# Kernel tuning notes

Measured on AMD Instinct MI355X. Metric: run time of the kernel, lower is better.

The kernel has to match this reference:

```python
import jax, jax.numpy as jnp
import numpy as np

B, M, N, K = 2, 25000, 100000, 16
HID, DIM, NGROUPS = 64, 64, 8
GN_EPS = 1e-5


def conv1x1(x, w, b):
    # x: [B,C,M,K], w: [O,C], b: [O]
    return jnp.einsum('bcmk,oc->bomk', x, w) + b[None, :, None, None]


def group_norm(x, gamma, beta, ngroups):
    b, c, m, k = x.shape
    xg = x.reshape(b, ngroups, c // ngroups, m, k)
    mu = xg.mean(axis=(2, 3, 4), keepdims=True)
    var = xg.var(axis=(2, 3, 4), keepdims=True)
    xn = ((xg - mu) / jnp.sqrt(var + GN_EPS)).reshape(b, c, m, k)
    return xn * gamma[None, :, None, None] + beta[None, :, None, None]


def mlp(x, w1, b1, g, be, w2, b2):
    h = jax.nn.relu(group_norm(conv1x1(x, w1, b1), g, be, NGROUPS))
    return conv1x1(h, w2, b2)


def setup_inputs() -> dict:
    key = jax.random.key(0)
    ks = jax.random.split(key, 16)
    inp = {
        'q_xyzs': jax.random.normal(ks[0], (B, 3, M), jnp.float32),
        'k_xyzs': jax.random.normal(ks[1], (B, 3, N), jnp.float32),
        'knn_idx': jax.random.randint(ks[2], (B, M, K), 0, N),
        'mask': jax.random.randint(ks[3], (B, M, K), 0, 2).astype(bool),
        # embed_positions MLP params
        'pe_w1': jax.random.normal(ks[4], (HID, 4), jnp.float32) * 0.05,
        'pe_b1': jnp.zeros((HID,), jnp.float32),
        'pe_g': jnp.ones((HID,), jnp.float32),
        'pe_be': jnp.zeros((HID,), jnp.float32),
        'pe_w2': jax.random.normal(ks[5], (DIM, HID), jnp.float32) * 0.05,
        'pe_b2': jnp.zeros((DIM,), jnp.float32),
        # attention MLP params
        'at_w1': jax.random.normal(ks[6], (HID, DIM), jnp.float32) * 0.05,
        'at_b1': jnp.zeros((HID,), jnp.float32),
        'at_g': jnp.ones((HID,), jnp.float32),
        'at_be': jnp.zeros((HID,), jnp.float32),
        'at_w2': jax.random.normal(ks[7], (DIM, HID), jnp.float32) * 0.05,
        'at_b2': jnp.zeros((DIM,), jnp.float32),
    }
    return inp


def reference(q_xyzs, k_xyzs, knn_idx, mask,
              pe_w1, pe_b1, pe_g, pe_be, pe_w2, pe_b2,
              at_w1, at_b1, at_g, at_be, at_w2, at_b2):
    # gather KNN coordinates: [B,3,M,K]
    knn_xyzs = jax.vmap(lambda pts, idx: pts[:, idx])(k_xyzs, knn_idx)
    offset = knn_xyzs - q_xyzs[..., None]
    dist = jnp.linalg.norm(offset, axis=1, keepdims=True)  # [B,1,M,K]
    direction = offset / jnp.maximum(dist, 1e-12)
    local_pattern = jnp.concatenate([direction, dist], axis=1)  # [B,4,M,K]

    pe = mlp(local_pattern, pe_w1, pe_b1, pe_g, pe_be, pe_w2, pe_b2)  # [B,DIM,M,K]
    attn = mlp(pe, at_w1, at_b1, at_g, at_be, at_w2, at_b2)
    mask_value = -jnp.finfo(attn.dtype).max
    attn = jnp.where(mask[:, None], attn, mask_value)
    attn = jax.nn.softmax(attn, axis=-1)
    return (pe * attn).sum(axis=-1)  # [B,DIM,M]
```

## Files before the change

### kernel.cpp

```cpp
#include <hip/hip_runtime.h>

#define Bn 2
#define Mn 25000
#define Nn 100000
#define MK 400000
#define GN_EPS 1e-5f
#define NEG_BIG (-3.402823466e+38f)
#define LOG2E 1.44269504088896340736f

#define G1 512
#define G2 512

#define BEFF_OFF 0
#define B1P_OFF  64
#define AB1P_OFF 192
#define AB2L_OFF 320
#define WF16_OFF 384
#define AW1P_OFF 6528
#define W1F_OFF  10624
#define MSK_OFF  11136
#define SP_OFF   36160
#define YP_OFF   52544
#define YS_OFF   183616
#define KXT_OFF  184128
#define QT_OFF   984128
#define XF_OFF   1184128

typedef _Float16 hf8 __attribute__((ext_vector_type(8)));
typedef _Float16 hf4 __attribute__((ext_vector_type(4)));
typedef _Float16 hf2 __attribute__((ext_vector_type(2)));
typedef float f32x16 __attribute__((ext_vector_type(16)));

__device__ __forceinline__ f32x16 mfma16(hf8 a, hf8 b, f32x16 c) {
    return __builtin_amdgcn_mfma_f32_32x32x16_f16(a, b, c, 0, 0, 0);
}
__device__ __forceinline__ f32x16 splat16(float v) {
    f32x16 x;
#pragma unroll
    for (int r = 0; r < 16; ++r) x[r] = v;
    return x;
}
__device__ __forceinline__ hf8 zero8() {
    hf8 z;
#pragma unroll
    for (int j = 0; j < 8; ++j) z[j] = (_Float16)0.f;
    return z;
}
__device__ __forceinline__ hf2 pkcvt(float a, float b) {
    return __builtin_bit_cast(hf2, __builtin_amdgcn_cvt_pkrtz(a, b));
}
__device__ __forceinline__ hf2 pkrelu(hf2 v) {
    hf2 z; z[0] = (_Float16)0.f; z[1] = (_Float16)0.f;
    return __builtin_elementwise_max(v, z);
}
__device__ __forceinline__ float waveSum(float v) {
#pragma unroll
    for (int s = 32; s; s >>= 1) v += __shfl_down(v, s, 64);
    return v;
}
#define ROWFN(r, lane) (((r) & 3) + 8*((r) >> 2) + 4*((lane) >> 5))

__global__ __launch_bounds__(256) void prep0_kernel(
    const float* __restrict__ q, const float* __restrict__ kx,
    float* __restrict__ ws)
{
    float4* kxt = (float4*)(ws + KXT_OFF);
    float4* qt  = (float4*)(ws + QT_OFF);
    for (int e = blockIdx.x*256 + threadIdx.x; e < 2*Nn; e += gridDim.x*256) {
        const int b = e / Nn, n = e % Nn;
        float4 v;
        v.x = kx[(b*3+0)*Nn + n]; v.y = kx[(b*3+1)*Nn + n];
        v.z = kx[(b*3+2)*Nn + n]; v.w = 0.f;
        kxt[e] = v;
    }
    for (int e = blockIdx.x*256 + threadIdx.x; e < 2*Mn; e += gridDim.x*256) {
        const int b = e / Mn, m = e % Mn;
        float4 v;
        v.x = q[(b*3+0)*Mn + m]; v.y = q[(b*3+1)*Mn + m];
        v.z = q[(b*3+2)*Mn + m]; v.w = 0.f;
        qt[e] = v;
    }
}

__global__ __launch_bounds__(256) void gatherx_kernel(
    const int* __restrict__ idx, const int* __restrict__ mask,
    float* __restrict__ ws)
{
    __shared__ float red[4][16];
    const int b = blockIdx.y;
    const float4* kxt = (const float4*)(ws + KXT_OFF) + (size_t)b*Nn;
    const float4* qt  = (const float4*)(ws + QT_OFF)  + (size_t)b*Mn;
    _Float16* xf = (_Float16*)(ws + XF_OFF);
    unsigned short* m16 = (unsigned short*)(ws + MSK_OFF) + (size_t)b*25024;
    float v[14];
#pragma unroll
    for (int j = 0; j < 14; ++j) v[j] = 0.f;

    for (int i = blockIdx.x*256 + threadIdx.x; i < MK; i += G1*256) {
        const int mm = i >> 4;
        const int id = idx[(size_t)b*MK + i];
        const float4 kv = kxt[id];
        const float4 qv = qt[mm];
        const float ox = kv.x - qv.x, oy = kv.y - qv.y, oz = kv.z - qv.z;
        const float d  = sqrtf(ox*ox + oy*oy + oz*oz);
        const float inv = 1.0f / fmaxf(d, 1e-12f);
        const float x0 = ox*inv, x1 = oy*inv, x2 = oz*inv, x3 = d;

        const hf2 lo = pkcvt(x0, x1);
        const hf2 hi = pkcvt(x2, x3);
        hf4 pk;
        pk[0] = lo[0]; pk[1] = lo[1]; pk[2] = hi[0]; pk[3] = hi[1];
        *(hf4*)&xf[((size_t)b*MK + i)*4] = pk;

        const unsigned long long mb = __ballot(mask[(size_t)b*MK + i] != 0);
        if ((threadIdx.x & 63) == 0)
            *(unsigned long long*)&m16[i >> 4] = mb;

        v[0] += x0; v[1] += x1; v[2] += x2; v[3] += x3;
        v[4] += x0*x0; v[5] += x0*x1; v[6] += x0*x2; v[7] += x0*x3;
        v[8] += x1*x1; v[9] += x1*x2; v[10] += x1*x3;
        v[11] += x2*x2; v[12] += x2*x3; v[13] += x3*x3;
    }
    const int lane = threadIdx.x & 63, wv = threadIdx.x >> 6;
#pragma unroll
    for (int j = 0; j < 14; ++j) v[j] = waveSum(v[j]);
    if (lane == 0) {
#pragma unroll
        for (int j = 0; j < 14; ++j) red[wv][j] = v[j];
    }
    __syncthreads();
    if (threadIdx.x < 14)
        ws[SP_OFF + ((size_t)b*G1 + blockIdx.x)*16 + threadIdx.x] =
            red[0][threadIdx.x] + red[1][threadIdx.x] + red[2][threadIdx.x] + red[3][threadIdx.x];
}

__global__ void prep1_kernel(
    const float* __restrict__ ws_r,
    const float* __restrict__ w1, const float* __restrict__ b1,
    const float* __restrict__ g1, const float* __restrict__ be1,
    const float* __restrict__ w2, const float* __restrict__ pe_b2,
    const float* __restrict__ aw1, const float* __restrict__ ab1,
    const float* __restrict__ aw2, const float* __restrict__ ab2,
    float* __restrict__ ws)
{
    const int t = threadIdx.x;
    _Float16* WF = (_Float16*)(ws + WF16_OFF);

    if (blockIdx.x > 0) {
        const int e = (blockIdx.x - 1)*256 + t;
        const int o = e >> 6, c = e & 63;
        WF[e]        = (_Float16)w2[e];
        WF[4096 + e] = (_Float16)(aw2[e] * LOG2E);
        float acc = 0.f;
        for (int d = 0; d < 64; ++d) acc = fmaf(aw1[o*64 + d], w2[d*64 + c], acc);
        WF[8192 + e] = (_Float16)acc;
        return;
    }

    __shared__ double S[2][14];
    __shared__ float Eh[2][64], Eq[2][64];

    if (t < 28) {
        const int b = t / 14, j = t % 14;
        const float* p = ws_r + SP_OFF + (size_t)b*G1*16 + j;
        double acc = 0.0;
        for (int g = 0; g < G1; g += 4)
            acc += (double)p[(g+0)*16] + (double)p[(g+1)*16]
                 + (double)p[(g+2)*16] + (double)p[(g+3)*16];
        S[b][j] = acc;
    }
    __syncthreads();

    if (t < 128) {
        const int b = t >> 6, o = t & 63;
        const double inv = 1.0 / (double)MK;
        double mu[4];
#pragma unroll
        for (int c = 0; c < 4; ++c) mu[c] = S[b][c] * inv;
        double m2[4][4];
        {
            const int map[4][4] = {{0,1,2,3},{1,4,5,6},{2,5,7,8},{3,6,8,9}};
#pragma unroll
            for (int c = 0; c < 4; ++c)
#pragma unroll
                for (int c2 = 0; c2 < 4; ++c2)
                    m2[c][c2] = S[b][4 + map[c][c2]] * inv;
        }
        double w[4];
#pragma unroll
        for (int c = 0; c < 4; ++c) w[c] = (double)w1[o*4 + c];
        double s = 0.0, qd = 0.0;
#pragma unroll
        for (int c = 0; c < 4; ++c) {
            s += w[c] * mu[c];
#pragma unroll
            for (int c2 = 0; c2 < 4; ++c2) qd += w[c]*w[c2]*m2[c][c2];
        }
        const double bb = (double)b1[o];
        Eh[b][o] = (float)(s + bb);
        Eq[b][o] = (float)(qd + 2.0*bb*s + bb*bb);
    }
    __syncthreads();
    if (t < 128) {
        const int b = t >> 6, o = t & 63, g = o & ~7;
        float mg = 0.f, qg = 0.f;
#pragma unroll
        for (int j = 0; j < 8; ++j) { mg += Eh[b][g + j]; qg += Eq[b][g + j]; }
        mg *= 0.125f; qg *= 0.125f;
        const float var = fmaxf(qg - mg*mg, 0.f);
        const float a = g1[o] / sqrtf(var + GN_EPS);
        const float c1v = be1[o] - mg*a;
        _Float16* W1F = (_Float16*)(ws + W1F_OFF);
        hf8 wrow;
#pragma unroll
        for (int c = 0; c < 4; ++c) wrow[c] = (_Float16)(a * w1[o*4 + c]);
#pragma unroll
        for (int c = 4; c < 8; ++c) wrow[c] = (_Float16)0.f;
        *(hf8*)&W1F[(b*64 + o)*8] = wrow;
        ws[B1P_OFF + b*64 + o] = fmaf(a, b1[o], c1v);
    }
    if (t < 64) {
        float acc = ab1[t];
        for (int d = 0; d < 64; ++d) acc = fmaf(aw1[t*64 + d], pe_b2[d], acc);
        ws[BEFF_OFF + t] = acc;
    } else if (t < 128) {
        ws[AB2L_OFF + (t - 64)] = ab2[t - 64] * LOG2E;
    }
}

__global__ __launch_bounds__(256, 4) void pass2_kernel(
    const float* __restrict__ cws, float* __restrict__ ws)
{
    __shared__ __align__(16) _Float16 Xs[4][32][72];
    const int b = blockIdx.y;
    const int tid = threadIdx.x, lane = tid & 63, wv = tid >> 6;
    const int colA = lane & 31;
    const int klo = (lane >> 5) * 8;
    const _Float16* xf  = (const _Float16*)(cws + XF_OFF);
    const _Float16* WFe = (const _Float16*)(cws + WF16_OFF) + 8192;
    const _Float16* W1F = (const _Float16*)(cws + W1F_OFF);

    hf8 BW[2][4];
#pragma unroll
    for (int jc = 0; jc < 2; ++jc)
#pragma unroll
        for (int ks = 0; ks < 4; ++ks)
            BW[jc][ks] = *(const hf8*)&WFe[(2*colA + jc)*64 + 16*ks + klo];
    hf8 BX[2];
    if (klo == 0) {
        BX[0] = *(const hf8*)&W1F[(b*64 + 2*colA)*8];
        BX[1] = *(const hf8*)&W1F[(b*64 + 2*colA + 1)*8];
    } else { BX[0] = zero8(); BX[1] = zero8(); }
    const float bias0 = cws[B1P_OFF + b*64 + 2*colA];
    const float bias1 = cws[B1P_OFF + b*64 + 2*colA + 1];

    float sh[2] = {0.f, 0.f}, sq[2] = {0.f, 0.f};

    for (int base = blockIdx.x * 128; base < MK; base += G2 * 128) {
        const int pt0 = base + 32*wv;
        hf8 ax = zero8();
        if (klo == 0) {
            hf4 xv = *(const hf4*)&xf[((size_t)b*MK + pt0 + colA)*4];
#pragma unroll
            for (int j = 0; j < 4; ++j) ax[j] = xv[j];
        }
        f32x16 r0 = splat16(bias0), r1t = splat16(bias1);
        r0  = mfma16(ax, BX[0], r0);
        r1t = mfma16(ax, BX[1], r1t);
#pragma unroll
        for (int r = 0; r < 16; ++r) {
            const int row = ROWFN(r, lane);
            *(hf2*)&Xs[wv][row][2*colA] = pkrelu(pkcvt(r0[r], r1t[r]));
        }
        hf8 A[4];
#pragma unroll
        for (int ks = 0; ks < 4; ++ks)
            A[ks] = *(const hf8*)&Xs[wv][colA][16*ks + klo];
#pragma unroll
        for (int jc = 0; jc < 2; ++jc) {
            f32x16 C = splat16(0.f);
#pragma unroll
            for (int ks = 0; ks < 4; ++ks) C = mfma16(A[ks], BW[jc][ks], C);
#pragma unroll
            for (int r = 0; r < 16; ++r) {
                const float vy = C[r];
                sh[jc] += vy;
                sq[jc] = fmaf(vy, vy, sq[jc]);
            }
        }
    }

#pragma unroll
    for (int jc = 0; jc < 2; ++jc) {
        sh[jc] += __shfl_xor(sh[jc], 32, 64);
        sq[jc] += __shfl_xor(sq[jc], 32, 64);
    }
    __syncthreads();
    float* red = (float*)Xs;
    if (lane < 32) {
#pragma unroll
        for (int jc = 0; jc < 2; ++jc) {
            red[wv*128 +      2*colA + jc] = sh[jc];
            red[wv*128 + 64 + 2*colA + jc] = sq[jc];
        }
    }
    __syncthreads();
    if (tid < 128) {
        const float v = red[tid] + red[128 + tid] + red[256 + tid] + red[384 + tid];
        ws[YP_OFF + ((size_t)b*G2 + blockIdx.x)*128 + tid] = v;
    }
}

__global__ __launch_bounds__(64) void prep2a_kernel(
    const float* __restrict__ ws_r, float* __restrict__ ws)
{
    const int o2 = blockIdx.x;
    const int b = o2 >> 7, i = o2 & 127;
    const float* p = ws_r + YP_OFF + (size_t)b*G2*128 + i;
    double acc = 0.0;
    for (int g = threadIdx.x; g < G2; g += 64) acc += (double)p[(size_t)g*128];
#pragma unroll
    for (int s = 32; s; s >>= 1) acc += __shfl_down(acc, s, 64);
    if (threadIdx.x == 0) ((double*)(ws + YS_OFF))[o2] = acc;
}

__global__ void prep2b_kernel(const float* __restrict__ ws_r,
                              const float* __restrict__ g2, const float* __restrict__ be2,
                              const float* __restrict__ aw1, const float* __restrict__ ab1,
                              float* __restrict__ ws)
{
    __shared__ float EH[2][64], EQ[2][64];
    __shared__ float A2s[2][64];
    const int t = threadIdx.x;
    const double* YS = (const double*)(ws_r + YS_OFF);
    if (t < 128) {
        const int b = t >> 6, o = t & 63;
        const double invMK = 1.0 / (double)MK;
        const double my = YS[b*128 + o] * invMK;
        const double qy = YS[b*128 + 64 + o] * invMK;
        const double beff = (double)ws_r[BEFF_OFF + o];
        EH[b][o] = (float)(my + beff);
        EQ[b][o] = (float)(qy + 2.0*beff*my + beff*beff);
    }
    __syncthreads();
    if (t < 128) {
        const int b = t >> 6, o = t & 63, g = o & ~7;
        float mg = 0.f, qg = 0.f;
#pragma unroll
        for (int j = 0; j < 8; ++j) { mg += EH[b][g + j]; qg += EQ[b][g + j]; }
        mg *= 0.125f; qg *= 0.125f;
        const float var = fmaxf(qg - mg*mg, 0.f);
        const float a = g2[o] / sqrtf(var + GN_EPS);
        A2s[b][o] = a;
        ws[AB1P_OFF + b*64 + o] = fmaf(a, ab1[o], be2[o] - mg*a);
    }
    __syncthreads();
    _Float16* AW1P = (_Float16*)(ws + AW1P_OFF);
    for (int e = t; e < 8192; e += 256) {
        const int b = e >> 12, oc = e & 4095, o = oc >> 6;
        AW1P[e] = (_Float16)(A2s[b][o] * aw1[oc]);
    }
}

__global__ __launch_bounds__(256, 3) void pass3_kernel(
    const float* __restrict__ b2,
    const float* __restrict__ cws, float* __restrict__ out)
{
    __shared__ __align__(16) _Float16 Xs[8][32][72];
    float* O = (float*)Xs;

    const int b = blockIdx.y;
    const int base = blockIdx.x * 256;
    const int tid = threadIdx.x;
    const int lane = tid & 63, wv = tid >> 6;
    const int colA = lane & 31;
    const int klo = (lane >> 5) * 8;

    const _Float16* xf   = (const _Float16*)(cws + XF_OFF);
    const _Float16* WF   = (const _Float16*)(cws + WF16_OFF);
    const _Float16* AW1P = (const _Float16*)(cws + AW1P_OFF) + (size_t)b*4096;
    const _Float16* W1F  = (const _Float16*)(cws + W1F_OFF);
    const unsigned short* m16 = (const unsigned short*)(cws + MSK_OFF) + (size_t)b*25024;

    int pt0[2];
    pt0[0] = base + 64*wv;
    pt0[1] = base + 64*wv + 32;
    unsigned mb[2];
#pragma unroll
    for (int t = 0; t < 2; ++t)
        mb[t] = (pt0[t] < MK) ? *(const unsigned*)(m16 + (pt0[t] >> 4)) : 0u;
    const unsigned mbs0 = __builtin_amdgcn_readfirstlane(mb[0]);
    const unsigned mbs1 = __builtin_amdgcn_readfirstlane(mb[1]);

    {
        hf8 BX0, BX1;
        if (klo == 0) {
            BX0 = *(const hf8*)&W1F[(b*64 + 2*colA)*8];
            BX1 = *(const hf8*)&W1F[(b*64 + 2*colA + 1)*8];
        } else { BX0 = zero8(); BX1 = zero8(); }
        const float bias0 = cws[B1P_OFF + b*64 + 2*colA];
        const float bias1 = cws[B1P_OFF + b*64 + 2*colA + 1];
#pragma unroll
        for (int t = 0; t < 2; ++t) {
            hf8 ax = zero8();
            if (klo == 0 && pt0[t] < MK) {
                hf4 xv = *(const hf4*)&xf[((size_t)b*MK + pt0[t] + colA)*4];
#pragma unroll
                for (int j = 0; j < 4; ++j) ax[j] = xv[j];
            }
            f32x16 r0 = splat16(bias0), r1t = splat16(bias1);
            r0  = mfma16(ax, BX0, r0);
            r1t = mfma16(ax, BX1, r1t);
#pragma unroll
            for (int r = 0; r < 16; ++r) {
                const int row = ROWFN(r, lane);
                *(hf2*)&Xs[2*wv + t][row][2*colA] = pkrelu(pkcvt(r0[r], r1t[r]));
            }
            if (lane < 32) {
                hf8 pad = zero8();
                pad[0] = ((mb[t] >> lane) & 1u) ? (_Float16)0.f : (_Float16)(-60000.f);
                *(hf8*)&Xs[2*wv + t][lane][64] = pad;
            }
        }
    }

    hf2 pe_pk[2][16];
    {
        f32x16 p00 = splat16(b2[2*colA]);
        f32x16 p01 = splat16(b2[2*colA + 1]);
        f32x16 p10 = p00, p11 = p01;
#pragma unroll
        for (int ks = 0; ks < 4; ++ks) {
            const int off = 16*ks + klo;
            hf8 a0  = *(const hf8*)&Xs[2*wv    ][colA][off];
            hf8 a1  = *(const hf8*)&Xs[2*wv + 1][colA][off];
            hf8 b0f = *(const hf8*)&WF[(2*colA)*64 + off];
            hf8 b1f = *(const hf8*)&WF[(2*colA + 1)*64 + off];
            p00 = mfma16(a0, b0f, p00);
            p01 = mfma16(a0, b1f, p01);
            p10 = mfma16(a1, b0f, p10);
            p11 = mfma16(a1, b1f, p11);
        }
#pragma unroll
        for (int r = 0; r < 16; ++r) {
            const int row = ROWFN(r, lane);
            pe_pk[0][r] = pkcvt(p00[r], p01[r]);
            pe_pk[1][r] = pkcvt(p10[r], p11[r]);
            *(hf2*)&Xs[2*wv    ][row][2*colA] = pe_pk[0][r];
            *(hf2*)&Xs[2*wv + 1][row][2*colA] = pe_pk[1][r];
        }
    }

    {
        f32x16 h00 = splat16(cws[AB1P_OFF + b*64 + 2*colA]);
        f32x16 h01 = splat16(cws[AB1P_OFF + b*64 + 2*colA + 1]);
        f32x16 h10 = h00, h11 = h01;
#pragma unroll
        for (int ks = 0; ks < 4; ++ks) {
            const int off = 16*ks + klo;
            hf8 a0  = *(const hf8*)&Xs[2*wv    ][colA][off];
            hf8 a1  = *(const hf8*)&Xs[2*wv + 1][colA][off];
            hf8 b0f = *(const hf8*)&AW1P[(2*colA)*64 + off];
            hf8 b1f = *(const hf8*)&AW1P[(2*colA + 1)*64 + off];
            h00 = mfma16(a0, b0f, h00);
            h01 = mfma16(a0, b1f, h01);
            h10 = mfma16(a1, b0f, h10);
            h11 = mfma16(a1, b1f, h11);
        }
#pragma unroll
        for (int r = 0; r < 16; ++r) {
            const int row = ROWFN(r, lane);
            *(hf2*)&Xs[2*wv    ][row][2*colA] = pkrelu(pkcvt(h00[r], h01[r]));
            *(hf2*)&Xs[2*wv + 1][row][2*colA] = pkrelu(pkcvt(h10[r], h11[r]));
        }
    }

    f32x16 l00 = splat16(cws[AB2L_OFF + 2*colA]);
    f32x16 l01 = splat16(cws[AB2L_OFF + 2*colA + 1]);
    f32x16 l10 = l00, l11 = l01;
#pragma unroll
    for (int ks = 0; ks < 4; ++ks) {
        const int off = 16*ks + klo;
        hf8 a0  = *(const hf8*)&Xs[2*wv    ][colA][off];
        hf8 a1  = *(const hf8*)&Xs[2*wv + 1][colA][off];
        hf8 b0f = *(const hf8*)&WF[4096 + (2*colA)*64 + off];
        hf8 b1f = *(const hf8*)&WF[4096 + (2*colA + 1)*64 + off];
        l00 = mfma16(a0, b0f, l00);
        l01 = mfma16(a0, b1f, l01);
        l10 = mfma16(a1, b0f, l10);
        l11 = mfma16(a1, b1f, l11);
    }
    {
        hf8 b5 = zero8();
        if (klo == 0) b5[0] = (_Float16)1.f;
        hf8 a50 = zero8(), a51 = zero8();
        if (klo == 0) {
            a50 = *(const hf8*)&Xs[2*wv    ][colA][64];
            a51 = *(const hf8*)&Xs[2*wv + 1][colA][64];
        }
        l00 = mfma16(a50, b5, l00);
        l01 = mfma16(a50, b5, l01);
        l10 = mfma16(a51, b5, l10);
        l11 = mfma16(a51, b5, l11);
    }

    __syncthreads();

    {
        auto softmax_tile = [&](const f32x16& lg, const hf2* pp, unsigned mbst,
                                int t, int j) {
#pragma unroll
            for (int mh = 0; mh < 2; ++mh) {
                float mx = lg[8*mh];
#pragma unroll
                for (int rr = 1; rr < 8; ++rr) mx = fmaxf(mx, lg[8*mh + rr]);
                mx = fmaxf(mx, __shfl_xor(mx, 32, 64));
                float se, sw = 0.f;
                if (((mbst >> (16*mh)) & 0xFFFFu) != 0u) {
                    se = 0.f;
#pragma unroll
                    for (int rr = 0; rr < 8; ++rr) {
                        const float e = exp2f(lg[8*mh + rr] - mx);
                        se += e;
                        sw = fmaf(e, (float)pp[8*mh + rr][j], sw);
                    }
                } else {
                    se = 8.f;
#pragma unroll
                    for (int rr = 0; rr < 8; ++rr) sw += (float)pp[8*mh + rr][j];
                }
                se += __shfl_xor(se, 32, 64);
                sw += __shfl_xor(sw, 32, 64);
                if (lane < 32)
                    O[(2*lane + j)*17 + (4*wv + 2*t + mh)] = sw * __builtin_amdgcn_rcpf(se);
            }
        };
        softmax_tile(l00, pe_pk[0], mbs0, 0, 0);
        softmax_tile(l01, pe_pk[0], mbs0, 0, 1);
        softmax_tile(l10, pe_pk[1], mbs1, 1, 0);
        softmax_tile(l11, pe_pk[1], mbs1, 1, 1);
    }
    __syncthreads();

    {
        const int o = tid >> 2, mq = (tid & 3) * 4;
        const int m0 = blockIdx.x * 16;
        if (m0 + mq < Mn) {
            float4 v;
            v.x = O[o*17 + mq];     v.y = O[o*17 + mq + 1];
            v.z = O[o*17 + mq + 2]; v.w = O[o*17 + mq + 3];
            *(float4*)&out[((size_t)b*64 + o)*Mn + m0 + mq] = v;
        }
    }
}

extern "C" void kernel_launch(void* const* d_in, const int* in_sizes, int n_in,
                              void* d_out, int out_size, void* d_ws, size_t ws_size,
                              hipStream_t stream) {
    (void)in_sizes; (void)n_in; (void)out_size; (void)ws_size;
    const float* q    = (const float*)d_in[0];
    const float* kx   = (const float*)d_in[1];
    const int*   idx  = (const int*)  d_in[2];
    const int*   mask = (const int*)  d_in[3];
    const float* w1   = (const float*)d_in[4];
    const float* b1   = (const float*)d_in[5];
    const float* g1   = (const float*)d_in[6];
    const float* be1  = (const float*)d_in[7];
    const float* w2   = (const float*)d_in[8];
    const float* b2   = (const float*)d_in[9];
    const float* aw1  = (const float*)d_in[10];
    const float* ab1  = (const float*)d_in[11];
    const float* g2   = (const float*)d_in[12];
    const float* be2  = (const float*)d_in[13];
    const float* aw2  = (const float*)d_in[14];
    const float* ab2  = (const float*)d_in[15];
    float* out = (float*)d_out;
    float* ws  = (float*)d_ws;

    prep0_kernel<<<256, 256, 0, stream>>>(q, kx, ws);
    gatherx_kernel<<<dim3(G1, Bn), 256, 0, stream>>>(idx, mask, ws);
    prep1_kernel<<<17, 256, 0, stream>>>(ws, w1, b1, g1, be1, w2, b2, aw1, ab1, aw2, ab2, ws);
    pass2_kernel<<<dim3(G2, Bn), 256, 0, stream>>>(ws, ws);
    prep2a_kernel<<<256, 64, 0, stream>>>(ws, ws);
    prep2b_kernel<<<1, 256, 0, stream>>>(ws, g2, be2, aw1, ab1, ws);
    pass3_kernel<<<dim3((MK + 255)/256, Bn), 256, 0, stream>>>(b2, ws, out);
}
```

Before: 193.5 us.

## Swizzle LDS tiles, apply mask in registers, raise occupancy, parallelize stat reduction

Pass3 drops the 72-wide padded LDS tile for a 64-wide tile with an XOR swizzle, removing the pad column. The mask is now applied directly to the logit registers using the wave-uniform mask bits, replacing the extra MFMA that added a mask column, which saves LDS and four MFMAs. Launch bounds go from 3 to 5 blocks per CU to allow higher occupancy, at the risk of register spills. The stats reduction in the prep kernel is spread across 224 threads with a shared-memory second stage instead of 28 serial threads.

```diff
diff --git a/kernel.cpp b/kernel.cpp
--- a/kernel.cpp
+++ b/kernel.cpp
@@ -7,6 +7,7 @@
 #define GN_EPS 1e-5f
 #define NEG_BIG (-3.402823466e+38f)
 #define LOG2E 1.44269504088896340736f
+#define MASK_NEG (-60000.f)
 
 #define G1 512
 #define G2 512
@@ -59,6 +60,7 @@
     return v;
 }
 #define ROWFN(r, lane) (((r) & 3) + 8*((r) >> 2) + 4*((lane) >> 5))
+#define SWZH(row, col) ((col) ^ ((((row) & 7)) << 3))
 
 __global__ __launch_bounds__(256) void prep0_kernel(
     const float* __restrict__ q, const float* __restrict__ kx,
@@ -158,16 +160,24 @@
     }
 
     __shared__ double S[2][14];
+    __shared__ double Sp[28][8];
     __shared__ float Eh[2][64], Eq[2][64];
 
+    if (t < 224) {
+        const int p = t >> 3, sub = t & 7;
+        const int b = p / 14, j = p % 14;
+        const float* src = ws_r + SP_OFF + (size_t)b*G1*16 + j;
+        double acc = 0.0;
+        for (int g = sub; g < G1; g += 8)
+            acc += (double)src[(size_t)g*16];
+        Sp[p][sub] = acc;
+    }
+    __syncthreads();
     if (t < 28) {
-        const int b = t / 14, j = t % 14;
-        const float* p = ws_r + SP_OFF + (size_t)b*G1*16 + j;
         double acc = 0.0;
-        for (int g = 0; g < G1; g += 4)
-            acc += (double)p[(g+0)*16] + (double)p[(g+1)*16]
-                 + (double)p[(g+2)*16] + (double)p[(g+3)*16];
-        S[b][j] = acc;
+#pragma unroll
+        for (int s = 0; s < 8; ++s) acc += Sp[t][s];
+        S[t / 14][t % 14] = acc;
     }
     __syncthreads();
 
@@ -362,11 +372,11 @@
     }
 }
 
-__global__ __launch_bounds__(256, 3) void pass3_kernel(
+__global__ __launch_bounds__(256, 5) void pass3_kernel(
     const float* __restrict__ b2,
     const float* __restrict__ cws, float* __restrict__ out)
 {
-    __shared__ __align__(16) _Float16 Xs[8][32][72];
+    __shared__ __align__(16) _Float16 Xs[8][32][64];
     float* O = (float*)Xs;
 
     const int b = blockIdx.y;
@@ -374,7 +384,8 @@
     const int tid = threadIdx.x;
     const int lane = tid & 63, wv = tid >> 6;
     const int colA = lane & 31;
-    const int klo = (lane >> 5) * 8;
+    const int hi = lane >> 5;
+    const int klo = hi * 8;
 
     const _Float16* xf   = (const _Float16*)(cws + XF_OFF);
     const _Float16* WF   = (const _Float16*)(cws + WF16_OFF);
@@ -414,12 +425,7 @@
 #pragma unroll
             for (int r = 0; r < 16; ++r) {
                 const int row = ROWFN(r, lane);
-                *(hf2*)&Xs[2*wv + t][row][2*colA] = pkrelu(pkcvt(r0[r], r1t[r]));
-            }
-            if (lane < 32) {
-                hf8 pad = zero8();
-                pad[0] = ((mb[t] >> lane) & 1u) ? (_Float16)0.f : (_Float16)(-60000.f);
-                *(hf8*)&Xs[2*wv + t][lane][64] = pad;
+                *(hf2*)&Xs[2*wv + t][row][SWZH(row, 2*colA)] = pkrelu(pkcvt(r0[r], r1t[r]));
             }
         }
     }
@@ -431,11 +437,11 @@
         f32x16 p10 = p00, p11 = p01;
 #pragma unroll
         for (int ks = 0; ks < 4; ++ks) {
-            const int off = 16*ks + klo;
+            const int off = SWZH(colA, 16*ks + klo);
             hf8 a0  = *(const hf8*)&Xs[2*wv    ][colA][off];
             hf8 a1  = *(const hf8*)&Xs[2*wv + 1][colA][off];
-            hf8 b0f = *(const hf8*)&WF[(2*colA)*64 + off];
-            hf8 b1f = *(const hf8*)&WF[(2*colA + 1)*64 + off];
+            hf8 b0f = *(const hf8*)&WF[(2*colA)*64 + 16*ks + klo];
+            hf8 b1f = *(const hf8*)&WF[(2*colA + 1)*64 + 16*ks + klo];
             p00 = mfma16(a0, b0f, p00);
             p01 = mfma16(a0, b1f, p01);
             p10 = mfma16(a1, b0f, p10);
@@ -446,8 +452,8 @@
             const int row = ROWFN(r, lane);
             pe_pk[0][r] = pkcvt(p00[r], p01[r]);
             pe_pk[1][r] = pkcvt(p10[r], p11[r]);
-            *(hf2*)&Xs[2*wv    ][row][2*colA] = pe_pk[0][r];
-            *(hf2*)&Xs[2*wv + 1][row][2*colA] = pe_pk[1][r];
+            *(hf2*)&Xs[2*wv    ][row][SWZH(row, 2*colA)] = pe_pk[0][r];
+            *(hf2*)&Xs[2*wv + 1][row][SWZH(row, 2*colA)] = pe_pk[1][r];
         }
     }
 
@@ -457,11 +463,11 @@
         f32x16 h10 = h00, h11 = h01;
 #pragma unroll
         for (int ks = 0; ks < 4; ++ks) {
-            const int off = 16*ks + klo;
+            const int off = SWZH(colA, 16*ks + klo);
             hf8 a0  = *(const hf8*)&Xs[2*wv    ][colA][off];
             hf8 a1  = *(const hf8*)&Xs[2*wv + 1][colA][off];
-            hf8 b0f = *(const hf8*)&AW1P[(2*colA)*64 + off];
-            hf8 b1f = *(const hf8*)&AW1P[(2*colA + 1)*64 + off];
+            hf8 b0f = *(const hf8*)&AW1P[(2*colA)*64 + 16*ks + klo];
+            hf8 b1f = *(const hf8*)&AW1P[(2*colA + 1)*64 + 16*ks + klo];
             h00 = mfma16(a0, b0f, h00);
             h01 = mfma16(a0, b1f, h01);
             h10 = mfma16(a1, b0f, h10);
@@ -470,8 +476,8 @@
 #pragma unroll
         for (int r = 0; r < 16; ++r) {
             const int row = ROWFN(r, lane);
-            *(hf2*)&Xs[2*wv    ][row][2*colA] = pkrelu(pkcvt(h00[r], h01[r]));
-            *(hf2*)&Xs[2*wv + 1][row][2*colA] = pkrelu(pkcvt(h10[r], h11[r]));
+            *(hf2*)&Xs[2*wv    ][row][SWZH(row, 2*colA)] = pkrelu(pkcvt(h00[r], h01[r]));
+            *(hf2*)&Xs[2*wv + 1][row][SWZH(row, 2*colA)] = pkrelu(pkcvt(h10[r], h11[r]));
         }
     }
 
@@ -480,28 +486,30 @@
     f32x16 l10 = l00, l11 = l01;
 #pragma unroll
     for (int ks = 0; ks < 4; ++ks) {
-        const int off = 16*ks + klo;
+        const int off = SWZH(colA, 16*ks + klo);
         hf8 a0  = *(const hf8*)&Xs[2*wv    ][colA][off];
         hf8 a1  = *(const hf8*)&Xs[2*wv + 1][colA][off];
-        hf8 b0f = *(const hf8*)&WF[4096 + (2*colA)*64 + off];
-        hf8 b1f = *(const hf8*)&WF[4096 + (2*colA + 1)*64 + off];
+        hf8 b0f = *(const hf8*)&WF[4096 + (2*colA)*64 + 16*ks + klo];
+        hf8 b1f = *(const hf8*)&WF[4096 + (2*colA + 1)*64 + 16*ks + klo];
         l00 = mfma16(a0, b0f, l00);
         l01 = mfma16(a0, b1f, l01);
         l10 = mfma16(a1, b0f, l10);
         l11 = mfma16(a1, b1f, l11);
     }
+
     {
-        hf8 b5 = zero8();
-        if (klo == 0) b5[0] = (_Float16)1.f;
-        hf8 a50 = zero8(), a51 = zero8();
-        if (klo == 0) {
-            a50 = *(const hf8*)&Xs[2*wv    ][colA][64];
-            a51 = *(const hf8*)&Xs[2*wv + 1][colA][64];
-        }
-        l00 = mfma16(a50, b5, l00);
-        l01 = mfma16(a50, b5, l01);
-        l10 = mfma16(a51, b5, l10);
-        l11 = mfma16(a51, b5, l11);
+        const unsigned msh0 = mbs0 >> (4*hi);
+        const unsigned msh1 = mbs1 >> (4*hi);
+#pragma unroll
+        for (int r = 0; r < 16; ++r) {
+            const int bit = (r & 3) + 8*(r >> 2);
+            const bool k0 = (msh0 >> bit) & 1u;
+            const bool k1 = (msh1 >> bit) & 1u;
+            l00[r] = k0 ? l00[r] : MASK_NEG;
+            l01[r] = k0 ? l01[r] : MASK_NEG;
+            l10[r] = k1 ? l10[r] : MASK_NEG;
+            l11[r] = k1 ? l11[r] : MASK_NEG;
+        }
     }
 
     __syncthreads();
```

After: 220.8 us. +14.1%, slower.

## Apply key mask with register selects instead of padded MFMA column

Applied to the files above, without the earlier changes.

Pass 3 no longer writes a mask pad column into shared memory and folds it in with four extra MFMAs. It now selects the logits directly in registers from the wave-uniform mask bits, putting the large negative value where keys are masked. Launch bounds rise from 3 to 4 blocks per SIMD to raise occupancy. The trade-off is register pressure: spills become possible, and the logits change from logit-plus-mask to a clamped constant, which softmax treats the same way.

```diff
diff --git a/kernel.cpp b/kernel.cpp
--- a/kernel.cpp
+++ b/kernel.cpp
@@ -7,6 +7,7 @@
 #define GN_EPS 1e-5f
 #define NEG_BIG (-3.402823466e+38f)
 #define LOG2E 1.44269504088896340736f
+#define MASK_NEG (-60000.f)
 
 #define G1 512
 #define G2 512
@@ -362,7 +363,7 @@
     }
 }
 
-__global__ __launch_bounds__(256, 3) void pass3_kernel(
+__global__ __launch_bounds__(256, 4) void pass3_kernel(
     const float* __restrict__ b2,
     const float* __restrict__ cws, float* __restrict__ out)
 {
@@ -374,7 +375,8 @@
     const int tid = threadIdx.x;
     const int lane = tid & 63, wv = tid >> 6;
     const int colA = lane & 31;
-    const int klo = (lane >> 5) * 8;
+    const int hi = lane >> 5;
+    const int klo = hi * 8;
 
     const _Float16* xf   = (const _Float16*)(cws + XF_OFF);
     const _Float16* WF   = (const _Float16*)(cws + WF16_OFF);
@@ -415,11 +417,6 @@
             for (int r = 0; r < 16; ++r) {
                 const int row = ROWFN(r, lane);
                 *(hf2*)&Xs[2*wv + t][row][2*colA] = pkrelu(pkcvt(r0[r], r1t[r]));
-            }
-            if (lane < 32) {
-                hf8 pad = zero8();
-                pad[0] = ((mb[t] >> lane) & 1u) ? (_Float16)0.f : (_Float16)(-60000.f);
-                *(hf8*)&Xs[2*wv + t][lane][64] = pad;
             }
         }
     }
@@ -490,18 +487,20 @@
         l10 = mfma16(a1, b0f, l10);
         l11 = mfma16(a1, b1f, l11);
     }
+
     {
-        hf8 b5 = zero8();
-        if (klo == 0) b5[0] = (_Float16)1.f;
-        hf8 a50 = zero8(), a51 = zero8();
-        if (klo == 0) {
-            a50 = *(const hf8*)&Xs[2*wv    ][colA][64];
-            a51 = *(const hf8*)&Xs[2*wv + 1][colA][64];
-        }
-        l00 = mfma16(a50, b5, l00);
-        l01 = mfma16(a50, b5, l01);
-        l10 = mfma16(a51, b5, l10);
-        l11 = mfma16(a51, b5, l11);
+        const unsigned msh0 = mbs0 >> (4*hi);
+        const unsigned msh1 = mbs1 >> (4*hi);
+#pragma unroll
+        for (int r = 0; r < 16; ++r) {
+            const int bit = (r & 3) + 8*(r >> 2);
+            const bool k0 = (msh0 >> bit) & 1u;
+            const bool k1 = (msh1 >> bit) & 1u;
+            l00[r] = k0 ? l00[r] : MASK_NEG;
+            l01[r] = k0 ? l01[r] : MASK_NEG;
+            l10[r] = k1 ? l10[r] : MASK_NEG;
+            l11[r] = k1 ? l11[r] : MASK_NEG;
+        }
     }
 
     __syncthreads();
```

Measured after the change: 194.5 us. Within noise of the previous version (+0.5%).
